# Optimization experiments

Measured on AMD Instinct MI355X. Metric: run time of the kernel, lower is better.

## Reference

```python
import jax, jax.numpy as jnp
import numpy as np


def setup_inputs() -> dict:
    key = jax.random.key(0)
    k1, k2 = jax.random.split(key)
    img_render_points = jax.random.normal(k1, (128, 128, 2), dtype=jnp.float32)
    ref_catheter_contour_point_cloud = jax.random.normal(k2, (16384, 2), dtype=jnp.float32)
    return {
        "img_render_points": img_render_points,
        "ref_catheter_contour_point_cloud": ref_catheter_contour_point_cloud,
    }


def reference(img_render_points, ref_catheter_contour_point_cloud):
    # Flatten to point cloud (N, 2)
    pc = img_render_points.reshape(-1, 2)
    ref = ref_catheter_contour_point_cloud  # (M, 2)
    # Pairwise Euclidean distances (N, M); torch.norm(..., dim=2) equivalent
    diff = pc[:, None, :] - ref[None, :, :]          # (N, M, 2)
    distances = jnp.sqrt(jnp.sum(diff * diff, axis=-1))  # (N, M)
    min_d1 = jnp.min(distances, axis=1)  # nearest ref point for each render point
    min_d2 = jnp.min(distances, axis=0)  # nearest render point for each ref point
    chamfer_loss = jnp.sum(min_d1) + jnp.sum(min_d2)
    return chamfer_loss
```

## Files before the change

### kernel.cpp

```cpp
#include <hip/hip_runtime.h>
#include <math.h>


#define NPTS  16384
#define BLK   512
#define QPB   64
#define NCH   16
#define CH    1024
#define SCALE 16.0f
#define INVS  0.0625f

typedef _Float16 f16x8 __attribute__((ext_vector_type(8)));
typedef float    f32x4 __attribute__((ext_vector_type(4)));


__device__ __forceinline__ void gload16(const void* g, void* l) {
    __builtin_amdgcn_global_load_lds(
        (const __attribute__((address_space(1))) unsigned int*)g,
        (__attribute__((address_space(3))) unsigned int*)l, 16, 0, 0);
}

__global__ __launch_bounds__(256) void cc_pack_kernel(
        const float2* __restrict__ pc, const float2* __restrict__ ref,
        f16x8* __restrict__ tbl, float* __restrict__ out) {
    int idx = blockIdx.x * 256 + threadIdx.x;
    if (idx == 0) out[0] = 0.0f;
    int dir = idx >> 14;
    int i   = idx & (NPTS - 1);
    float2 t = dir ? pc[i] : ref[i];
    float xs = t.x * SCALE, ys = t.y * SCALE;
    _Float16 hx = (_Float16)xs; _Float16 lx = (_Float16)(xs - (float)hx);
    _Float16 hy = (_Float16)ys; _Float16 ly = (_Float16)(ys - (float)hy);
    float zz = fmaf(xs, xs, ys * ys);
    _Float16 hz = (_Float16)zz; _Float16 lz = (_Float16)(zz - (float)hz);
    f16x8 p;
    p[0] = (_Float16)(-2.0f * (float)hx);
    p[1] = (_Float16)(-2.0f * (float)lx);
    p[2] = p[0];
    p[3] = (_Float16)(-2.0f * (float)hy);
    p[4] = (_Float16)(-2.0f * (float)ly);
    p[5] = p[3];
    p[6] = hz;
    p[7] = lz;
    tbl[idx] = p;
}

__global__ __launch_bounds__(BLK, 4) void cc_min_kernel(
        const float2* __restrict__ pc, const float2* __restrict__ ref,
        const f16x8* __restrict__ tbl, float* __restrict__ out) {
    __shared__ f16x8 stage[2][2 * CH];
    __shared__ f32x4 xbuf[4][64];
    __shared__ float psum[16];

    const int b    = blockIdx.x;
    const int dir  = b >> 8;
    const int qblk = b & 255;
    const int tid  = threadIdx.x;
    const int w    = tid >> 6;
    const int lane = tid & 63;
    const int half = w >> 2;
    const int qt   = w & 3;

    const float2* __restrict__ qry = dir ? ref : pc;
    const f16x8*  __restrict__ tb  = tbl + dir * NPTS;

    const int q0 = qblk * QPB + qt * 16;
    f16x8 A;
#pragma unroll
    for (int e = 0; e < 8; ++e) A[e] = (_Float16)0.0f;
    if (lane < 16) {
        float2 qp = qry[q0 + lane];
        float xs = qp.x * SCALE, ys = qp.y * SCALE;
        _Float16 hx = (_Float16)xs; _Float16 lx = (_Float16)(xs - (float)hx);
        _Float16 hy = (_Float16)ys; _Float16 ly = (_Float16)(ys - (float)hy);
        A[0] = hx; A[1] = hx; A[2] = lx;
        A[3] = hy; A[4] = hy; A[5] = ly;
        A[6] = (_Float16)1.0f; A[7] = (_Float16)1.0f;
    }

    const int lo = w * 1024;
#define STAGE(buf, c)                                                        \
    {                                                                        \
        const char* g0 = (const char*)(tb + (c) * CH);                       \
        const char* g1 = (const char*)(tb + (8 + (c)) * CH);                 \
        char* lb = (char*)&stage[buf][0];                                    \
        gload16(g0 + lo + lane * 16,          lb + lo);                      \
        gload16(g0 + lo + 8192 + lane * 16,   lb + lo + 8192);               \
        gload16(g1 + lo + lane * 16,          lb + lo + 16384);              \
        gload16(g1 + lo + 8192 + lane * 16,   lb + lo + 24576);              \
    }

    f32x4 m = (f32x4){INFINITY, INFINITY, INFINITY, INFINITY};
    const f32x4 Z4 = (f32x4){0.f, 0.f, 0.f, 0.f};
    const int bo = lane & 15;

    STAGE(0, 0);
    __syncthreads();

    for (int c = 0; c < 8; ++c) {
        if (c < 7) STAGE((c + 1) & 1, c + 1);
        const f16x8* S = &stage[c & 1][half * CH];
#pragma unroll 8
        for (int tt = 0; tt < 64; tt += 2) {
            f16x8 b0 = S[tt * 16 + bo];
            f16x8 b1 = S[tt * 16 + 16 + bo];
            f32x4 d0 = __builtin_amdgcn_mfma_f32_16x16x32_f16(A, b0, Z4, 0, 0, 0);
            f32x4 d1 = __builtin_amdgcn_mfma_f32_16x16x32_f16(A, b1, Z4, 0, 0, 0);
#pragma unroll
            for (int r = 0; r < 4; ++r)
                m[r] = fminf(fminf(m[r], d0[r]), d1[r]);
        }
        __syncthreads();
    }

    if (half) *(f32x4*)&xbuf[qt][lane] = m;
    __syncthreads();
    if (!half) {
        f32x4 o = *(const f32x4*)&xbuf[qt][lane];
#pragma unroll
        for (int r = 0; r < 4; ++r) m[r] = fminf(m[r], o[r]);

#pragma unroll
        for (int r = 0; r < 4; ++r) {
            float v = m[r];
            v = fminf(v, __shfl_xor(v, 1, 16));
            v = fminf(v, __shfl_xor(v, 2, 16));
            v = fminf(v, __shfl_xor(v, 4, 16));
            v = fminf(v, __shfl_xor(v, 8, 16));
            m[r] = v;
        }

        if ((lane & 15) == 0) {
            int g = lane >> 4;
            float ssum = 0.0f;
#pragma unroll
            for (int r = 0; r < 4; ++r) {
                float2 qp = qry[q0 + g * 4 + r];
                float xs = qp.x * SCALE, ys = qp.y * SCALE;
                float pn = fmaf(xs, xs, ys * ys);
                ssum += sqrtf(fmaxf(m[r] + pn, 0.0f));
            }
            psum[w * 4 + g] = ssum;
        }
    }
    __syncthreads();
    if (tid == 0) {
        float t = 0.0f;
#pragma unroll
        for (int k = 0; k < 16; ++k) t += psum[k];
        atomicAdd(out, t * INVS);
    }
}

extern "C" void kernel_launch(void* const* d_in, const int* in_sizes, int n_in,
                              void* d_out, int out_size, void* d_ws, size_t ws_size,
                              hipStream_t stream) {
    const float2* pc  = (const float2*)d_in[0];
    const float2* ref = (const float2*)d_in[1];
    float* out = (float*)d_out;
    f16x8* tbl = (f16x8*)d_ws;

    cc_pack_kernel<<<(2 * NPTS) / 256, 256, 0, stream>>>(pc, ref, tbl, out);
    cc_min_kernel<<<512, BLK, 0, stream>>>(pc, ref, tbl, out);
}
```

Baseline: 85.08 us.

## Switch min-distance kernel to 32x32x16 MFMA with two query tiles per wave

Replaces the 16x16x32 MFMA tiling, where waves split queries into four 16-row tiles and reference points into two halves, with 32x32x16 MFMA. Every wave now covers all 64 queries as two 32-row tiles over its own slice of each staged 2048-point chunk. Each B fragment loaded from LDS is reused across both query tiles, which is meant to cut LDS reads and instruction overhead per distance. Because all eight waves hold partial minima for the same queries, the final cross-wave min reduction now goes through a swizzled LDS arena. The larger f32x16 accumulators raise register pressure under the 4-blocks-per-CU launch bound.

```diff
diff --git a/kernel.cpp b/kernel.cpp
--- a/kernel.cpp
+++ b/kernel.cpp
@@ -5,13 +5,13 @@
 #define NPTS  16384
 #define BLK   512
 #define QPB   64
-#define NCH   16
-#define CH    1024
+#define NCHK  8
+#define CHT   2048
 #define SCALE 16.0f
 #define INVS  0.0625f
 
-typedef _Float16 f16x8 __attribute__((ext_vector_type(8)));
-typedef float    f32x4 __attribute__((ext_vector_type(4)));
+typedef _Float16 f16x8  __attribute__((ext_vector_type(8)));
+typedef float    f32x16 __attribute__((ext_vector_type(16)));
 
 
 __device__ __forceinline__ void gload16(const void* g, void* l) {
@@ -48,9 +48,8 @@
 __global__ __launch_bounds__(BLK, 4) void cc_min_kernel(
         const float2* __restrict__ pc, const float2* __restrict__ ref,
         const f16x8* __restrict__ tbl, float* __restrict__ out) {
-    __shared__ f16x8 stage[2][2 * CH];
-    __shared__ f32x4 xbuf[4][64];
-    __shared__ float psum[16];
+    __shared__ char arena[2 * CHT * 16];
+    __shared__ float psum[64];
 
     const int b    = blockIdx.x;
     const int dir  = b >> 8;
@@ -58,97 +57,109 @@
     const int tid  = threadIdx.x;
     const int w    = tid >> 6;
     const int lane = tid & 63;
-    const int half = w >> 2;
-    const int qt   = w & 3;
 
     const float2* __restrict__ qry = dir ? ref : pc;
     const f16x8*  __restrict__ tb  = tbl + dir * NPTS;
 
-    const int q0 = qblk * QPB + qt * 16;
-    f16x8 A;
+    const int q0 = qblk * QPB;
+    f16x8 A[2];
 #pragma unroll
-    for (int e = 0; e < 8; ++e) A[e] = (_Float16)0.0f;
-    if (lane < 16) {
-        float2 qp = qry[q0 + lane];
-        float xs = qp.x * SCALE, ys = qp.y * SCALE;
-        _Float16 hx = (_Float16)xs; _Float16 lx = (_Float16)(xs - (float)hx);
-        _Float16 hy = (_Float16)ys; _Float16 ly = (_Float16)(ys - (float)hy);
-        A[0] = hx; A[1] = hx; A[2] = lx;
-        A[3] = hy; A[4] = hy; A[5] = ly;
-        A[6] = (_Float16)1.0f; A[7] = (_Float16)1.0f;
+    for (int qt = 0; qt < 2; ++qt) {
+        f16x8 a;
+#pragma unroll
+        for (int e = 0; e < 8; ++e) a[e] = (_Float16)0.0f;
+        if (lane < 32) {
+            float2 qp = qry[q0 + qt * 32 + lane];
+            float xs = qp.x * SCALE, ys = qp.y * SCALE;
+            _Float16 hx = (_Float16)xs; _Float16 lx = (_Float16)(xs - (float)hx);
+            _Float16 hy = (_Float16)ys; _Float16 ly = (_Float16)(ys - (float)hy);
+            a[0] = hx; a[1] = hx; a[2] = lx;
+            a[3] = hy; a[4] = hy; a[5] = ly;
+            a[6] = (_Float16)1.0f; a[7] = (_Float16)1.0f;
+        }
+        A[qt] = a;
     }
 
-    const int lo = w * 1024;
 #define STAGE(buf, c)                                                        \
     {                                                                        \
-        const char* g0 = (const char*)(tb + (c) * CH);                       \
-        const char* g1 = (const char*)(tb + (8 + (c)) * CH);                 \
-        char* lb = (char*)&stage[buf][0];                                    \
-        gload16(g0 + lo + lane * 16,          lb + lo);                      \
-        gload16(g0 + lo + 8192 + lane * 16,   lb + lo + 8192);               \
-        gload16(g1 + lo + lane * 16,          lb + lo + 16384);              \
-        gload16(g1 + lo + 8192 + lane * 16,   lb + lo + 24576);              \
+        const char* gsrc = (const char*)tb + (size_t)(c) * (CHT * 16);       \
+        char* ldst = arena + (buf) * (CHT * 16);                             \
+        _Pragma("unroll")                                                    \
+        for (int k = 0; k < 4; ++k)                                          \
+            gload16(gsrc + k * 8192 + w * 1024 + lane * 16,                  \
+                    ldst + k * 8192 + w * 1024);                             \
     }
 
-    f32x4 m = (f32x4){INFINITY, INFINITY, INFINITY, INFINITY};
-    const f32x4 Z4 = (f32x4){0.f, 0.f, 0.f, 0.f};
-    const int bo = lane & 15;
+    f32x16 m[2];
+#pragma unroll
+    for (int qt = 0; qt < 2; ++qt)
+#pragma unroll
+        for (int r = 0; r < 16; ++r) m[qt][r] = INFINITY;
+    const f32x16 Z = {};
+    const int bo = lane & 31;
 
     STAGE(0, 0);
     __syncthreads();
 
-    for (int c = 0; c < 8; ++c) {
-        if (c < 7) STAGE((c + 1) & 1, c + 1);
-        const f16x8* S = &stage[c & 1][half * CH];
-#pragma unroll 8
-        for (int tt = 0; tt < 64; tt += 2) {
-            f16x8 b0 = S[tt * 16 + bo];
-            f16x8 b1 = S[tt * 16 + 16 + bo];
-            f32x4 d0 = __builtin_amdgcn_mfma_f32_16x16x32_f16(A, b0, Z4, 0, 0, 0);
-            f32x4 d1 = __builtin_amdgcn_mfma_f32_16x16x32_f16(A, b1, Z4, 0, 0, 0);
+    for (int c = 0; c < NCHK; ++c) {
+        if (c < NCHK - 1) STAGE((c + 1) & 1, c + 1);
+        const f16x8* S = (const f16x8*)(arena + (c & 1) * (CHT * 16));
 #pragma unroll
-            for (int r = 0; r < 4; ++r)
-                m[r] = fminf(fminf(m[r], d0[r]), d1[r]);
+        for (int i = 0; i < 8; i += 2) {
+            f16x8 b0 = S[(w * 8 + i) * 32 + bo];
+            f16x8 b1 = S[(w * 8 + i + 1) * 32 + bo];
+#pragma unroll
+            for (int qt = 0; qt < 2; ++qt) {
+                f32x16 d0 = __builtin_amdgcn_mfma_f32_32x32x16_f16(A[qt], b0, Z, 0, 0, 0);
+                f32x16 d1 = __builtin_amdgcn_mfma_f32_32x32x16_f16(A[qt], b1, Z, 0, 0, 0);
+#pragma unroll
+                for (int r = 0; r < 16; ++r)
+                    m[qt][r] = fminf(fminf(m[qt][r], d0[r]), d1[r]);
+            }
         }
         __syncthreads();
     }
 
-    if (half) *(f32x4*)&xbuf[qt][lane] = m;
+    float* red = (float*)arena;
+    {
+        const int wsw = w ^ ((lane >> 2) & 7);
+#pragma unroll
+        for (int qt = 0; qt < 2; ++qt)
+#pragma unroll
+            for (int r = 0; r < 16; ++r)
+                red[((qt * 16 + r) * 64 + lane) * 8 + wsw] = m[qt][r];
+    }
     __syncthreads();
-    if (!half) {
-        f32x4 o = *(const f32x4*)&xbuf[qt][lane];
+
+    {
+        int g = tid >> 3, sub = tid & 7;
+        int qt = g >> 5, r = (g >> 1) & 15, hi = g & 1;
+        const float4* base =
+            (const float4*)&red[((qt * 16 + r) * 64 + hi * 32 + sub * 4) * 8];
+        float v = INFINITY;
 #pragma unroll
-        for (int r = 0; r < 4; ++r) m[r] = fminf(m[r], o[r]);
-
-#pragma unroll
-        for (int r = 0; r < 4; ++r) {
-            float v = m[r];
-            v = fminf(v, __shfl_xor(v, 1, 16));
-            v = fminf(v, __shfl_xor(v, 2, 16));
-            v = fminf(v, __shfl_xor(v, 4, 16));
-            v = fminf(v, __shfl_xor(v, 8, 16));
-            m[r] = v;
+        for (int t = 0; t < 8; ++t) {
+            float4 x = base[t];
+            v = fminf(v, fminf(fminf(x.x, x.y), fminf(x.z, x.w)));
         }
-
-        if ((lane & 15) == 0) {
-            int g = lane >> 4;
-            float ssum = 0.0f;
-#pragma unroll
-            for (int r = 0; r < 4; ++r) {
-                float2 qp = qry[q0 + g * 4 + r];
-                float xs = qp.x * SCALE, ys = qp.y * SCALE;
-                float pn = fmaf(xs, xs, ys * ys);
-                ssum += sqrtf(fmaxf(m[r] + pn, 0.0f));
-            }
-            psum[w * 4 + g] = ssum;
+        v = fminf(v, __shfl_xor(v, 1, 64));
+        v = fminf(v, __shfl_xor(v, 2, 64));
+        v = fminf(v, __shfl_xor(v, 4, 64));
+        if (sub == 0) {
+            int row = (r & 3) + 8 * (r >> 2) + 4 * hi;
+            float2 qp = qry[q0 + qt * 32 + row];
+            float xs = qp.x * SCALE, ys = qp.y * SCALE;
+            float pn = fmaf(xs, xs, ys * ys);
+            psum[g] = sqrtf(fmaxf(v + pn, 0.0f));
         }
     }
     __syncthreads();
-    if (tid == 0) {
-        float t = 0.0f;
+    if (w == 0) {
+        float s = psum[lane];
 #pragma unroll
-        for (int k = 0; k < 16; ++k) t += psum[k];
-        atomicAdd(out, t * INVS);
+        for (int off = 32; off > 0; off >>= 1)
+            s += __shfl_down(s, off, 64);
+        if (lane == 0) atomicAdd(out, s * INVS);
     }
 }
 
```

Result: slower. 120.1 us (+41.1%).
